# Performance work log

Measured on AMD Instinct MI355X. Metric: run time of the kernel, lower is better.

The kernel has to match this reference:

```python
import jax, jax.numpy as jnp
import numpy as np

B, T, E = 2, 4096, 768
H = 12
WIN = 256  # one-sided window w; band width = 2w+1


def setup_inputs() -> dict:
    key = jax.random.key(0)
    k1, k2, k3, k4 = jax.random.split(key, 4)
    scale = 1.0 / np.sqrt(E)
    return {
        "x": jax.random.normal(k1, (B, T, E), dtype=jnp.float32),
        "Wq": jax.random.normal(k2, (E, E), dtype=jnp.float32) * scale,
        "Wk": jax.random.normal(k3, (E, E), dtype=jnp.float32) * scale,
        "Wv": jax.random.normal(k4, (E, E), dtype=jnp.float32) * scale,
    }


def reference(x, Wq, Wk, Wv):
    b, t, e = x.shape
    h, w = H, WIN
    s = e // h
    Wb = 2 * w + 1          # band width
    nc = t // w             # number of query chunks of size w

    # projections (nn.Linear, bias=False): y = x @ W^T
    q = (x @ Wq.T).reshape(b, t, h, s) * (1.0 / np.sqrt(s))
    k = (x @ Wk.T).reshape(b, t, h, s)
    v = (x @ Wv.T).reshape(b, t, h, s)

    # overlapping key/value chunks: chunk c covers absolute keys [c*w - w, c*w + 2w)
    pad = [(0, 0), (w, w), (0, 0), (0, 0)]
    kp = jnp.pad(k, pad).reshape(b, nc + 2, w, h, s)
    k3 = jnp.concatenate([kp[:, :-2], kp[:, 1:-1], kp[:, 2:]], axis=2)  # [b,nc,3w,h,s]
    vp = jnp.pad(v, pad).reshape(b, nc + 2, w, h, s)
    v3 = jnp.concatenate([vp[:, :-2], vp[:, 1:-1], vp[:, 2:]], axis=2)  # [b,nc,3w,h,s]

    qc = q.reshape(b, nc, w, h, s)
    scores = jnp.einsum('bcxhd,bcyhd->bhcxy', qc, k3)  # [b,h,nc,w,3w]

    # extract the banded diagonals: band j <-> key index p + j in the 3w window
    idx = jnp.arange(w)[:, None] + jnp.arange(Wb)[None, :]  # [w, 2w+1], values in [0,3w)
    band = jnp.take_along_axis(scores, idx[None, None, None], axis=-1)  # [b,h,nc,w,2w+1]
    band = band.reshape(b, h, t, Wb).transpose(0, 2, 1, 3)  # [b,t,h,2w+1]

    # mask_invalid_locations: key absolute pos = i + j - w must lie in [0, t)
    key_pos = jnp.arange(t)[:, None] + jnp.arange(Wb)[None, :] - w
    invalid = (key_pos < 0) | (key_pos >= t)
    band = jnp.where(invalid[None, :, None, :], -jnp.inf, band)

    probs = jax.nn.softmax(band.astype(jnp.float32), axis=-1).astype(x.dtype)

    # sliding_chunks_matmul_pv: scatter band probs back to the 3w window layout
    pc = probs.transpose(0, 2, 1, 3).reshape(b, h, nc, w, Wb)
    pc_pad = jnp.pad(pc, [(0, 0)] * 4 + [(w - 1, w - 1)])  # last axis len 4w-1
    # full[p, m] = band[p, m - p] for m-p in [0, 2w], else 0
    idx2 = (jnp.arange(3 * w)[None, :] - jnp.arange(w)[:, None]) + (w - 1)  # [w, 3w]
    pfull = jnp.take_along_axis(pc_pad, idx2[None, None, None], axis=-1)  # [b,h,nc,w,3w]

    out = jnp.einsum('bhcpm,bcmhd->bcphd', pfull, v3).reshape(b, t, e)
    return out
```

## Files before the change

kernel.cpp:

```cpp
#include <hip/hip_runtime.h>

#define B_ 2
#define T_ 4096
#define E_ 768
#define H_ 12
#define S_ 64
#define WIN_ 256

typedef unsigned short u16;
typedef unsigned int u32;
typedef __attribute__((ext_vector_type(8))) short bf16x8;
typedef __attribute__((ext_vector_type(4))) short bf16x4;
typedef __attribute__((ext_vector_type(4))) float f32x4;

__device__ __forceinline__ u16 f2bf(float f) {
  u32 u = __float_as_uint(f);
  u += ((u >> 16) & 1u) + 0x7fffu;
  return (u16)(u >> 16);
}

__device__ __forceinline__ void async_copy16(const u16* g, u16* l) {
  __builtin_amdgcn_global_load_lds(
      (const __attribute__((address_space(1))) void*)g,
      (__attribute__((address_space(3))) void*)l, 16, 0, 0);
}

__global__ void cvt_all(const float* __restrict__ x, const float* __restrict__ wq,
                        const float* __restrict__ wk, const float* __restrict__ wv,
                        u16* __restrict__ xb, u16* __restrict__ wb) {
  const int n4x = B_ * T_ * E_ / 4;
  const int n4w = E_ * E_ / 4;
  int i = blockIdx.x * 256 + threadIdx.x;
  const float* src;
  u16* dst;
  int j;
  if (i < n4x) {
    src = x; dst = xb; j = i;
  } else {
    int t = i - n4x;
    int z = t / n4w;
    if (z >= 3) return;
    j = t - z * n4w;
    src = (z == 0) ? wq : ((z == 1) ? wk : wv);
    dst = wb + (size_t)z * E_ * E_;
  }
  float4 v = ((const float4*)src)[j];
  ushort4 o;
  o.x = f2bf(v.x); o.y = f2bf(v.y); o.z = f2bf(v.z); o.w = f2bf(v.w);
  ((ushort4*)dst)[j] = o;
}

__global__ __launch_bounds__(256, 2)
void gemm_qkv(const u16* __restrict__ xb, const u16* __restrict__ wb,
              u16* __restrict__ qkv) {
  const int M = B_ * T_;
  __shared__ u16 As[4][128][8];
  __shared__ u16 Bs[4][128][8];
  int tid = threadIdx.x;
  int lane = tid & 63, wave = tid >> 6;
  int wr = wave >> 1, wc = wave & 1;
  int q8 = lane >> 4, nl = lane & 15;
  int bm = blockIdx.x * 128, bn = blockIdx.y * 128;
  int z = blockIdx.z;
  const u16* A = xb;
  const u16* Bmat = wb + (size_t)z * E_ * E_;
  u16* C = qkv + (size_t)z * M * E_;
  float scale = (z == 0) ? (0.125f * 1.44269504088896f) : 1.0f;

  f32x4 acc[4][4] = {};
  for (int k0 = 0; k0 < E_; k0 += 32) {
    __syncthreads();
#pragma unroll
    for (int j = 0; j < 2; ++j) {
      int u = tid + j * 256;
      int ch = u >> 7, row = u & 127;
      async_copy16(A + (size_t)(bm + row) * E_ + k0 + ch * 8, &As[ch][row][0]);
      async_copy16(Bmat + (size_t)(bn + row) * E_ + k0 + ch * 8, &Bs[ch][row][0]);
    }
    __syncthreads();
    bf16x8 af[4], bfr[4];
#pragma unroll
    for (int i = 0; i < 4; ++i)
      af[i] = *(const bf16x8*)&As[q8][wr * 64 + i * 16 + nl][0];
#pragma unroll
    for (int i = 0; i < 4; ++i)
      bfr[i] = *(const bf16x8*)&Bs[q8][wc * 64 + i * 16 + nl][0];
#pragma unroll
    for (int i = 0; i < 4; ++i)
#pragma unroll
      for (int j2 = 0; j2 < 4; ++j2)
        acc[i][j2] = __builtin_amdgcn_mfma_f32_16x16x32_bf16(af[i], bfr[j2], acc[i][j2], 0, 0, 0);
  }
#pragma unroll
  for (int i = 0; i < 4; ++i)
#pragma unroll
    for (int j2 = 0; j2 < 4; ++j2)
#pragma unroll
      for (int r = 0; r < 4; ++r) {
        int row = bm + wr * 64 + i * 16 + q8 * 4 + r;
        int col = bn + wc * 64 + j2 * 16 + nl;
        C[(size_t)row * E_ + col] = f2bf(acc[i][j2][r] * scale);
      }
}

__global__ void transpose_v(const u16* __restrict__ v, u16* __restrict__ vT) {
  __shared__ u16 lt[64][66];
  int t = threadIdx.x;
  int t0 = blockIdx.x * 64;
  int e0 = blockIdx.y * 64;
  int b = blockIdx.z;
#pragma unroll
  for (int i = 0; i < 2; ++i) {
    int u = t + i * 256;
    int tok = u >> 3, cg = u & 7;
    bf16x8 val = *(const bf16x8*)(v + (size_t)(b * T_ + t0 + tok) * E_ + e0 + cg * 8);
#pragma unroll
    for (int j = 0; j < 8; ++j) lt[tok][cg * 8 + j] = (u16)val[j];
  }
  __syncthreads();
#pragma unroll
  for (int i = 0; i < 2; ++i) {
    int u = t + i * 256;
    int d = u >> 3, ck = u & 7;
    bf16x8 o;
#pragma unroll
    for (int j = 0; j < 8; ++j) o[j] = (short)lt[ck * 8 + j][d];
    *(bf16x8*)(vT + (size_t)(b * E_ + e0 + d) * T_ + t0 + ck * 8) = o;
  }
}

__global__ __launch_bounds__(256, 2)
void attn_kernel(const u16* __restrict__ qkv, const u16* __restrict__ vT,
                 float* __restrict__ out) {
  const int Mtot = B_ * T_;
  const u16* qb = qkv;
  const u16* kb = qkv + (size_t)Mtot * E_;

  __shared__ u16 Pl[4][2][16][36];

  int tid = threadIdx.x;
  int lane = tid & 63, wave = tid >> 6;
  int q8 = lane >> 4, nl = lane & 15;
  int qs = blockIdx.x * 128;
  int bh = blockIdx.y;
  int b = bh / H_, h = bh % H_;
  int qw = qs + wave * 32;
  size_t ho = (size_t)h * S_;

  bf16x8 aq[2][2];
#pragma unroll
  for (int mt = 0; mt < 2; ++mt) {
    const u16* qrow = qb + (size_t)(b * T_ + qw + mt * 16 + nl) * E_ + ho;
    aq[mt][0] = *(const bf16x8*)(qrow + q8 * 8);
    aq[mt][1] = *(const bf16x8*)(qrow + 32 + q8 * 8);
  }

  f32x4 O[2][4] = {};
  f32x4 lacc[2] = {};

  int klo = qw - WIN_; if (klo < 0) klo = 0;
  int khi = qw + 32 + WIN_; if (khi > T_) khi = T_;

  const u16* kbase = kb + (size_t)b * T_ * E_ + ho;
  const u16* vbase = vT + (size_t)b * E_ * T_ + ho * T_;

  for (int kt = klo; kt < khi; kt += 32) {
    bf16x8 bk[2][2];
#pragma unroll
    for (int nt = 0; nt < 2; ++nt) {
      const u16* krow = kbase + (size_t)(kt + nt * 16 + nl) * E_;
      bk[nt][0] = *(const bf16x8*)(krow + q8 * 8);
      bk[nt][1] = *(const bf16x8*)(krow + 32 + q8 * 8);
    }

    f32x4 sc[2][2] = {};
#pragma unroll
    for (int nt = 0; nt < 2; ++nt)
#pragma unroll
      for (int mt = 0; mt < 2; ++mt) {
        sc[mt][nt] = __builtin_amdgcn_mfma_f32_16x16x32_bf16(aq[mt][0], bk[nt][0], sc[mt][nt], 0, 0, 0);
        sc[mt][nt] = __builtin_amdgcn_mfma_f32_16x16x32_bf16(aq[mt][1], bk[nt][1], sc[mt][nt], 0, 0, 0);
      }

    if (kt < qw - 225 || kt > qw + 225) {
#pragma unroll
      for (int mt = 0; mt < 2; ++mt)
#pragma unroll
        for (int nt = 0; nt < 2; ++nt)
#pragma unroll
          for (int r = 0; r < 4; ++r) {
            int qa = qw + mt * 16 + q8 * 4 + r;
            int ka = kt + nt * 16 + nl;
            int d = ka - qa;
            sc[mt][nt][r] = (d < -WIN_ || d > WIN_) ? -1e30f : sc[mt][nt][r];
          }
    }

#pragma unroll
    for (int mt = 0; mt < 2; ++mt)
#pragma unroll
      for (int r = 0; r < 4; ++r) {
        float p0 = exp2f(sc[mt][0][r]);
        float p1 = exp2f(sc[mt][1][r]);
        sc[mt][0][r] = p0; sc[mt][1][r] = p1;
        lacc[mt][r] += p0 + p1;
      }

#pragma unroll
    for (int mt = 0; mt < 2; ++mt)
#pragma unroll
      for (int r = 0; r < 4; ++r) {
        Pl[wave][mt][q8 * 4 + r][nl] = f2bf(sc[mt][0][r]);
        Pl[wave][mt][q8 * 4 + r][16 + nl] = f2bf(sc[mt][1][r]);
      }

    bf16x8 ap[2];
#pragma unroll
    for (int mt = 0; mt < 2; ++mt) {
      bf16x4 lo = *(const bf16x4*)&Pl[wave][mt][nl][q8 * 8];
      bf16x4 hi = *(const bf16x4*)&Pl[wave][mt][nl][q8 * 8 + 4];
      bf16x8 a;
      a[0] = lo[0]; a[1] = lo[1]; a[2] = lo[2]; a[3] = lo[3];
      a[4] = hi[0]; a[5] = hi[1]; a[6] = hi[2]; a[7] = hi[3];
      ap[mt] = a;
    }

#pragma unroll
    for (int dt = 0; dt < 4; ++dt) {
      bf16x8 bv = *(const bf16x8*)(vbase + (size_t)(dt * 16 + nl) * T_ + kt + q8 * 8);
#pragma unroll
      for (int mt = 0; mt < 2; ++mt)
        O[mt][dt] = __builtin_amdgcn_mfma_f32_16x16x32_bf16(ap[mt], bv, O[mt][dt], 0, 0, 0);
    }
  }

#pragma unroll
  for (int mt = 0; mt < 2; ++mt)
#pragma unroll
    for (int r = 0; r < 4; ++r) {
      float l = lacc[mt][r];
      l += __shfl_xor(l, 1); l += __shfl_xor(l, 2);
      l += __shfl_xor(l, 4); l += __shfl_xor(l, 8);
      float inv = 1.0f / l;
      int qa = qw + mt * 16 + q8 * 4 + r;
      float* op = out + (size_t)(b * T_ + qa) * E_ + ho;
#pragma unroll
      for (int dt = 0; dt < 4; ++dt)
        op[dt * 16 + nl] = O[mt][dt][r] * inv;
    }
}

extern "C" void kernel_launch(void* const* d_in, const int* in_sizes, int n_in,
                              void* d_out, int out_size, void* d_ws, size_t ws_size,
                              hipStream_t stream) {
  const float* x  = (const float*)d_in[0];
  const float* Wq = (const float*)d_in[1];
  const float* Wk = (const float*)d_in[2];
  const float* Wv = (const float*)d_in[3];
  float* out = (float*)d_out;

  const size_t M = (size_t)B_ * T_;
  u16* xb  = (u16*)d_ws;
  u16* wb  = xb + M * E_;
  u16* qkv = wb + 3 * (size_t)E_ * E_;
  u16* vT  = xb;

  const int n4x = B_ * T_ * E_ / 4;
  const int n4w = E_ * E_ / 4;
  int cvt_blocks = (n4x + 3 * n4w + 255) / 256;
  cvt_all<<<cvt_blocks, 256, 0, stream>>>(x, Wq, Wk, Wv, xb, wb);

  dim3 g1(M / 128, E_ / 128, 3);
  gemm_qkv<<<g1, 256, 0, stream>>>(xb, wb, qkv);

  dim3 gt(T_ / 64, E_ / 64, B_);
  transpose_v<<<gt, 256, 0, stream>>>(qkv + 2 * M * E_, vT);

  dim3 g2(T_ / 128, B_ * H_);
  attn_kernel<<<g2, 256, 0, stream>>>(qkv, vT, out);
}
```

Baseline: 215.2 us.

## Double-buffer GEMM LDS tiles and prefetch next K/V tiles in attention

```diff
diff --git a/kernel.cpp b/kernel.cpp
--- a/kernel.cpp
+++ b/kernel.cpp
@@ -50,12 +50,12 @@
   ((ushort4*)dst)[j] = o;
 }
 
-__global__ __launch_bounds__(256, 2)
+__global__ __launch_bounds__(256)
 void gemm_qkv(const u16* __restrict__ xb, const u16* __restrict__ wb,
               u16* __restrict__ qkv) {
   const int M = B_ * T_;
-  __shared__ u16 As[4][128][8];
-  __shared__ u16 Bs[4][128][8];
+  __shared__ u16 As[2][4][128][8];
+  __shared__ u16 Bs[2][4][128][8];
   int tid = threadIdx.x;
   int lane = tid & 63, wave = tid >> 6;
   int wr = wave >> 1, wc = wave & 1;
@@ -67,24 +67,39 @@
   u16* C = qkv + (size_t)z * M * E_;
   float scale = (z == 0) ? (0.125f * 1.44269504088896f) : 1.0f;
 
+  int ch0 = tid >> 7, row0 = tid & 127;
+  int u1 = tid + 256;
+  int ch1 = u1 >> 7, row1 = u1 & 127;
+  const u16* ga0 = A + (size_t)(bm + row0) * E_ + ch0 * 8;
+  const u16* ga1 = A + (size_t)(bm + row1) * E_ + ch1 * 8;
+  const u16* gb0 = Bmat + (size_t)(bn + row0) * E_ + ch0 * 8;
+  const u16* gb1 = Bmat + (size_t)(bn + row1) * E_ + ch1 * 8;
+
+  const int NK = E_ / 32;
+  async_copy16(ga0, &As[0][ch0][row0][0]);
+  async_copy16(ga1, &As[0][ch1][row1][0]);
+  async_copy16(gb0, &Bs[0][ch0][row0][0]);
+  async_copy16(gb1, &Bs[0][ch1][row1][0]);
+
   f32x4 acc[4][4] = {};
-  for (int k0 = 0; k0 < E_; k0 += 32) {
+  for (int ki = 0; ki < NK; ++ki) {
+    int buf = ki & 1;
     __syncthreads();
-#pragma unroll
-    for (int j = 0; j < 2; ++j) {
-      int u = tid + j * 256;
-      int ch = u >> 7, row = u & 127;
-      async_copy16(A + (size_t)(bm + row) * E_ + k0 + ch * 8, &As[ch][row][0]);
-      async_copy16(Bmat + (size_t)(bn + row) * E_ + k0 + ch * 8, &Bs[ch][row][0]);
-    }
-    __syncthreads();
+    if (ki + 1 < NK) {
+      int nb = buf ^ 1;
+      int koff = (ki + 1) * 32;
+      async_copy16(ga0 + koff, &As[nb][ch0][row0][0]);
+      async_copy16(ga1 + koff, &As[nb][ch1][row1][0]);
+      async_copy16(gb0 + koff, &Bs[nb][ch0][row0][0]);
+      async_copy16(gb1 + koff, &Bs[nb][ch1][row1][0]);
+    }
     bf16x8 af[4], bfr[4];
 #pragma unroll
     for (int i = 0; i < 4; ++i)
-      af[i] = *(const bf16x8*)&As[q8][wr * 64 + i * 16 + nl][0];
+      af[i] = *(const bf16x8*)&As[buf][q8][wr * 64 + i * 16 + nl][0];
 #pragma unroll
     for (int i = 0; i < 4; ++i)
-      bfr[i] = *(const bf16x8*)&Bs[q8][wc * 64 + i * 16 + nl][0];
+      bfr[i] = *(const bf16x8*)&Bs[buf][q8][wc * 64 + i * 16 + nl][0];
 #pragma unroll
     for (int i = 0; i < 4; ++i)
 #pragma unroll
@@ -129,7 +144,7 @@
   }
 }
 
-__global__ __launch_bounds__(256, 2)
+__global__ __launch_bounds__(256)
 void attn_kernel(const u16* __restrict__ qkv, const u16* __restrict__ vT,
                  float* __restrict__ out) {
   const int Mtot = B_ * T_;
@@ -164,13 +179,27 @@
   const u16* kbase = kb + (size_t)b * T_ * E_ + ho;
   const u16* vbase = vT + (size_t)b * E_ * T_ + ho * T_;
 
+  bf16x8 bk[2][2];
+#pragma unroll
+  for (int nt = 0; nt < 2; ++nt) {
+    const u16* krow = kbase + (size_t)(klo + nt * 16 + nl) * E_;
+    bk[nt][0] = *(const bf16x8*)(krow + q8 * 8);
+    bk[nt][1] = *(const bf16x8*)(krow + 32 + q8 * 8);
+  }
+
   for (int kt = klo; kt < khi; kt += 32) {
-    bf16x8 bk[2][2];
+    bf16x8 bv[4];
+#pragma unroll
+    for (int dt = 0; dt < 4; ++dt)
+      bv[dt] = *(const bf16x8*)(vbase + (size_t)(dt * 16 + nl) * T_ + kt + q8 * 8);
+
+    int ktn = (kt + 32 < khi) ? kt + 32 : kt;
+    bf16x8 nbk[2][2];
 #pragma unroll
     for (int nt = 0; nt < 2; ++nt) {
-      const u16* krow = kbase + (size_t)(kt + nt * 16 + nl) * E_;
-      bk[nt][0] = *(const bf16x8*)(krow + q8 * 8);
-      bk[nt][1] = *(const bf16x8*)(krow + 32 + q8 * 8);
+      const u16* krow = kbase + (size_t)(ktn + nt * 16 + nl) * E_;
+      nbk[nt][0] = *(const bf16x8*)(krow + q8 * 8);
+      nbk[nt][1] = *(const bf16x8*)(krow + 32 + q8 * 8);
     }
 
     f32x4 sc[2][2] = {};
@@ -226,11 +255,15 @@
     }
 
 #pragma unroll
-    for (int dt = 0; dt < 4; ++dt) {
-      bf16x8 bv = *(const bf16x8*)(vbase + (size_t)(dt * 16 + nl) * T_ + kt + q8 * 8);
+    for (int dt = 0; dt < 4; ++dt)
 #pragma unroll
       for (int mt = 0; mt < 2; ++mt)
-        O[mt][dt] = __builtin_amdgcn_mfma_f32_16x16x32_bf16(ap[mt], bv, O[mt][dt], 0, 0, 0);
+        O[mt][dt] = __builtin_amdgcn_mfma_f32_16x16x32_bf16(ap[mt], bv[dt], O[mt][dt], 0, 0, 0);
+
+#pragma unroll
+    for (int nt = 0; nt < 2; ++nt) {
+      bk[nt][0] = nbk[nt][0];
+      bk[nt][1] = nbk[nt][1];
     }
   }
 
```

New measurement: 211.0 us. 1.02x faster.
